# Kernel tuning notes

Measured on AMD Instinct MI355X. Metric: run time of the kernel, lower is better.

## Reference

```python
import jax, jax.numpy as jnp
import numpy as np

B, S, D = 2, 2048, 2048
NH, NKV, HD = 16, 4, 128  # num_heads, num_key_value_heads, head_dim

def setup_inputs() -> dict:
    key = jax.random.key(0)
    ks = jax.random.split(key, 5)
    sc = 0.02
    return {
        "hidden_states": jax.random.normal(ks[0], (B, S, D), jnp.float32),
        "Wq": jax.random.normal(ks[1], (NH * HD, D), jnp.float32) * sc,
        "Wk": jax.random.normal(ks[2], (NKV * HD, D), jnp.float32) * sc,
        "Wv": jax.random.normal(ks[3], (NKV * HD, D), jnp.float32) * sc,
        "Wo": jax.random.normal(ks[4], (D, NH * HD), jnp.float32) * sc,
    }

def reference(hidden_states, Wq, Wk, Wv, Wo):
    b, s, d = hidden_states.shape
    # projections (LLaMA linear: x @ W.T)
    q = jnp.einsum('bsd,ed->bse', hidden_states, Wq).reshape(b, s, NH, HD).transpose(0, 2, 1, 3)
    k = jnp.einsum('bsd,ed->bse', hidden_states, Wk).reshape(b, s, NKV, HD).transpose(0, 2, 1, 3)
    v = jnp.einsum('bsd,ed->bse', hidden_states, Wv).reshape(b, s, NKV, HD).transpose(0, 2, 1, 3)
    # GQA: repeat kv heads
    n_rep = NH // NKV
    k = jnp.repeat(k, n_rep, axis=1)  # [b, NH, s, HD]
    v = jnp.repeat(v, n_rep, axis=1)
    scale = 1.0 / jnp.sqrt(jnp.asarray(HD, hidden_states.dtype))
    scores = jnp.einsum('bhqd,bhkd->bhqk', q, k) * scale
    causal = jnp.tril(jnp.ones((s, s), bool))
    scores = jnp.where(causal, scores, jnp.asarray(-jnp.inf, scores.dtype))
    attn = jax.nn.softmax(scores, axis=-1)
    out = jnp.einsum('bhqk,bhkd->bhqd', attn, v)  # [b, NH, s, HD]
    out = out.transpose(0, 2, 1, 3).reshape(b, s, NH * HD)
    return jnp.einsum('bse,de->bsd', out, Wo)
```

## Files before the change

kernel.cpp:

```cpp
#include <hip/hip_runtime.h>

typedef unsigned short u16;
typedef unsigned int u32;
typedef __attribute__((ext_vector_type(4))) float f32x4;
typedef __attribute__((ext_vector_type(16))) float f32x16;
typedef __attribute__((ext_vector_type(8))) short bf16x8;


__device__ __forceinline__ u16 f2b(float f) {
  u32 u = __builtin_bit_cast(u32, f);
  u = (u + 0x7fffu + ((u >> 16) & 1u)) >> 16;
  return (u16)u;
}

__device__ __forceinline__ void gload_lds16(const void* g, void* l) {
  __builtin_amdgcn_global_load_lds((const __attribute__((address_space(1))) u32*)g,
                                   (__attribute__((address_space(3))) u32*)l, 16, 0, 0);
}

#if __has_builtin(__builtin_amdgcn_permlane32_swap)
#define HAS_PLS 1
__device__ __forceinline__ void pls(u32 x, u32 y, u32& rx, u32& ry) {
  auto r = __builtin_amdgcn_permlane32_swap(x, y, false, false);
  rx = (u32)r[0];
  ry = (u32)r[1];
}
#endif

__device__ __forceinline__ float xhalf_max(float v) {
#ifdef HAS_PLS
  u32 a, b;
  pls(__builtin_bit_cast(u32, v), __builtin_bit_cast(u32, v), a, b);
  return fmaxf(__builtin_bit_cast(float, a), __builtin_bit_cast(float, b));
#else
  return fmaxf(v, __shfl_xor(v, 32));
#endif
}

__device__ __forceinline__ float xhalf_sum(float v) {
#ifdef HAS_PLS
  u32 a, b;
  pls(__builtin_bit_cast(u32, v), __builtin_bit_cast(u32, v), a, b);
  return __builtin_bit_cast(float, a) + __builtin_bit_cast(float, b);
#else
  return v + __shfl_xor(v, 32);
#endif
}

__device__ __forceinline__ void xexchange(int hi, u32 a0, u32 a1, u32 a2, u32 a3, u32* o) {
#ifdef HAS_PLS
  pls(a0, a2, o[0], o[2]);
  pls(a1, a3, o[1], o[3]);
#else
  u32 xa0 = (u32)__shfl_xor((int)a0, 32), xa1 = (u32)__shfl_xor((int)a1, 32);
  u32 xa2 = (u32)__shfl_xor((int)a2, 32), xa3 = (u32)__shfl_xor((int)a3, 32);
  o[0] = hi ? xa2 : a0;
  o[1] = hi ? xa3 : a1;
  o[2] = hi ? a2 : xa0;
  o[3] = hi ? a3 : xa1;
#endif
}

__device__ __forceinline__ u32 pktrunc(float lo, float hif) {
  return (__builtin_bit_cast(u32, lo) >> 16) | (__builtin_bit_cast(u32, hif) & 0xffff0000u);
}

__global__ void cvt_bf16(const float* __restrict__ src, u16* __restrict__ dst, int n) {
  int stride = gridDim.x * blockDim.x * 4;
  for (int idx = (blockIdx.x * blockDim.x + threadIdx.x) * 4; idx < n; idx += stride) {
    float4 v = *(const float4*)(src + idx);
    ushort4 o;
    o.x = f2b(v.x); o.y = f2b(v.y); o.z = f2b(v.z); o.w = f2b(v.w);
    *(ushort4*)(dst + idx) = o;
  }
}

__global__ void cvt_w4(const float* __restrict__ Wq, const float* __restrict__ Wk,
                       const float* __restrict__ Wv, const float* __restrict__ Wo,
                       u16* __restrict__ dst) {
  const int total = 10485760;
  int stride = gridDim.x * blockDim.x * 4;
  for (int idx = (blockIdx.x * blockDim.x + threadIdx.x) * 4; idx < total; idx += stride) {
    const float* src;
    int off;
    if (idx < 4194304) { src = Wq; off = idx; }
    else if (idx < 5242880) { src = Wk; off = idx - 4194304; }
    else if (idx < 6291456) { src = Wv; off = idx - 5242880; }
    else { src = Wo; off = idx - 6291456; }
    float4 v = *(const float4*)(src + off);
    ushort4 o;
    o.x = f2b(v.x); o.y = f2b(v.y); o.z = f2b(v.z); o.w = f2b(v.w);
    *(ushort4*)(dst + idx) = o;
  }
}

template<int OUT_MODE>
__global__ __launch_bounds__(256) void gemm_bt(const u16* __restrict__ A, const u16* __restrict__ B,
                                               void* __restrict__ Cout, int M, int N, int Kd,
                                               u16* __restrict__ Kout, u16* __restrict__ Vtout) {
  __shared__ u16 smem[(OUT_MODE == 3) ? 16384 : 8192];
  u16* sA = smem;
  u16* sB = smem + 4096;
  const int tid = threadIdx.x;
  const int l = tid & 63, w = tid >> 6;
  const int wr = w >> 1, wc = w & 1;
  const int g = l >> 4, c = l & 15;
  const int tm = blockIdx.y * 128, tn = blockIdx.x * 128;

  f32x4 acc[4][4] = {};

  const int r0 = tid >> 2, cc = (tid & 3) << 3;

  for (int k0 = 0; k0 < Kd; k0 += 32) {
    __syncthreads();
    {
      const u16* srcA0 = A + (size_t)(tm + r0) * Kd + k0 + cc;
      const u16* srcB0 = B + (size_t)(tn + r0) * Kd + k0 + cc;
      gload_lds16(srcA0, (char*)sA + w * 1024);
      gload_lds16(srcB0, (char*)sB + w * 1024);
      gload_lds16(srcA0 + (size_t)64 * Kd, (char*)sA + 4096 + w * 1024);
      gload_lds16(srcB0 + (size_t)64 * Kd, (char*)sB + 4096 + w * 1024);
    }
    __syncthreads();

    bf16x8 af[4], bfr[4];
#pragma unroll
    for (int m = 0; m < 4; ++m)
      af[m] = *(const bf16x8*)(sA + (wr * 64 + m * 16 + c) * 32 + g * 8);
#pragma unroll
    for (int n = 0; n < 4; ++n)
      bfr[n] = *(const bf16x8*)(sB + (wc * 64 + n * 16 + c) * 32 + g * 8);
#pragma unroll
    for (int m = 0; m < 4; ++m)
#pragma unroll
      for (int n = 0; n < 4; ++n)
        acc[m][n] = __builtin_amdgcn_mfma_f32_16x16x32_bf16(af[m], bfr[n], acc[m][n], 0, 0, 0);
  }

  if constexpr (OUT_MODE == 3) {
    if (tn >= 2048) {
      const bool isK = tn < 2560;
      __syncthreads();
#pragma unroll
      for (int m = 0; m < 4; ++m)
#pragma unroll
        for (int n = 0; n < 4; ++n)
#pragma unroll
          for (int i = 0; i < 4; ++i) {
            int lr = wr * 64 + m * 16 + g * 4 + i;
            int lc = wc * 64 + n * 16 + c;
            int off;
            if (isK)
              off = ((lr >> 5) << 12) + ((lc >> 4) << 9) + (((lc >> 3) & 1) << 8) +
                    ((lr & 31) << 3) + (lc & 7);
            else
              off = ((lr >> 5) << 12) + (((lr >> 4) & 1) << 11) + ((lc >> 5) << 9) +
                    (((lr >> 3) & 1) << 8) + ((lc & 31) << 3) + (lr & 7);
            smem[off] = f2b(acc[m][n][i]);
          }
      __syncthreads();
      const int e0 = tn - (isK ? 2048 : 2560);
      const int bb = tm >> 11;
      u16* dstbase = (isK ? Kout : Vtout) +
                     ((((size_t)(bb * 4 + (e0 >> 7)) * 64 + ((tm & 2047) >> 5))) << 12);
#pragma unroll
      for (int ps = 0; ps < 8; ++ps) {
        int idx = ps * 2048 + tid * 8;
        *(bf16x8*)(dstbase + idx) = *(const bf16x8*)(smem + idx);
      }
      return;
    }
  }

#pragma unroll
  for (int m = 0; m < 4; ++m)
#pragma unroll
    for (int n = 0; n < 4; ++n)
#pragma unroll
      for (int i = 0; i < 4; ++i) {
        int row = tm + wr * 64 + m * 16 + g * 4 + i;
        int col = tn + wc * 64 + n * 16 + c;
        float v = acc[m][n][i];
        if constexpr (OUT_MODE == 2) {
          ((float*)Cout)[(size_t)row * N + col] = v;
        } else {
          ((u16*)Cout)[(size_t)row * 2048 + col] = f2b(v);
        }
      }
}

__global__ __launch_bounds__(256, 2) void attn_fwd(const u16* __restrict__ Q, const u16* __restrict__ Kf,
                                                   const u16* __restrict__ Vf, u16* __restrict__ AO) {
  const int l = threadIdx.x & 63, w = threadIdx.x >> 6;
  const int ql = l & 31, hi = l >> 5;
  const int bh = blockIdx.y;
  const int b = bh >> 4, h = bh & 15;
  const int kvh = h >> 2;

  __shared__ float4 mO[2][16][64];
  __shared__ float mML[2][2][64];

  const float sm = 0.08838834764831845f * 1.4426950408889634f;

  const u16* Kfb = Kf + (size_t)(b * 4 + kvh) * 64 * 4096 + l * 8;
  const u16* Vfb = Vf + (size_t)(b * 4 + kvh) * 64 * 4096 + l * 8;

  const int x = (int)blockIdx.x;

#define LOADK(KF, KV0)                                                        \
  do {                                                                        \
    const u16* kb_ = Kfb + (size_t)((KV0) >> 5) * 4096;                       \
    _Pragma("unroll") for (int ck = 0; ck < 8; ++ck)                          \
        KF[ck] = *(const bf16x8*)(kb_ + ck * 512);                            \
  } while (0)

#define COMPUTE(KF, KV0)                                                      \
  do {                                                                        \
    bf16x8 vtf[2][4];                                                         \
    {                                                                         \
      const u16* vb_ = Vfb + (size_t)((KV0) >> 5) * 4096;                     \
      _Pragma("unroll") for (int ks = 0; ks < 2; ++ks)                        \
      _Pragma("unroll") for (int db = 0; db < 4; ++db)                        \
          vtf[ks][db] = *(const bf16x8*)(vb_ + (ks * 4 + db) * 512);          \
    }                                                                         \
    f32x16 sacc = {};                                                         \
    __builtin_amdgcn_s_setprio(1);                                            \
    _Pragma("unroll") for (int ck = 0; ck < 8; ++ck)                          \
        sacc = __builtin_amdgcn_mfma_f32_32x32x16_bf16(KF[ck], qf[ck], sacc, 0, 0, 0); \
    __builtin_amdgcn_s_setprio(0);                                            \
    if ((KV0) == q0) {                             \
      _Pragma("unroll") for (int r = 0; r < 16; ++r) {                        \
        int crow = (r & 3) + 8 * (r >> 2) + 4 * hi;                           \
        if (crow > ql) sacc[r] = -1e30f;                                      \
      }                                                                       \
    }                                                                         \
    float t0 = fmaxf(sacc[0], sacc[1]), t1 = fmaxf(sacc[2], sacc[3]);         \
    float t2 = fmaxf(sacc[4], sacc[5]), t3 = fmaxf(sacc[6], sacc[7]);         \
    float t4 = fmaxf(sacc[8], sacc[9]), t5 = fmaxf(sacc[10], sacc[11]);       \
    float t6 = fmaxf(sacc[12], sacc[13]), t7 = fmaxf(sacc[14], sacc[15]);     \
    float mx = fmaxf(fmaxf(fmaxf(t0, t1), fmaxf(t2, t3)),                     \
                     fmaxf(fmaxf(t4, t5), fmaxf(t6, t7)));                    \
    mx = xhalf_max(mx);                                                       \
    float p[16];                                                              \
    _Pragma("unroll") for (int r = 0; r < 16; ++r)                            \
        p[r] = exp2f((sacc[r] - mrow) * sm);                                  \
    if (!__all((mx - mrow) * sm <= 8.0f)) {                \
      float mnew = fmaxf(mrow, mx);                                           \
      float rs = exp2f((mrow - mnew) * sm);                                   \
      mrow = mnew;                                                            \
      lrow *= rs;                                                             \
      _Pragma("unroll") for (int db = 0; db < 4; ++db)                        \
      _Pragma("unroll") for (int r = 0; r < 16; ++r) acc[db][r] *= rs;        \
      _Pragma("unroll") for (int r = 0; r < 16; ++r)                          \
          p[r] = exp2f((sacc[r] - mrow) * sm);                                \
    }                                                                         \
    float s0 = p[0] + p[1], s1 = p[2] + p[3], s2 = p[4] + p[5], s3 = p[6] + p[7]; \
    float s4 = p[8] + p[9], s5 = p[10] + p[11], s6 = p[12] + p[13], s7 = p[14] + p[15]; \
    float psum = ((s0 + s1) + (s2 + s3)) + ((s4 + s5) + (s6 + s7));           \
    lrow += xhalf_sum(psum);                                                  \
    u32 a0 = pktrunc(p[0], p[1]), a1 = pktrunc(p[2], p[3]);                   \
    u32 a2 = pktrunc(p[4], p[5]), a3 = pktrunc(p[6], p[7]);                   \
    u32 b0 = pktrunc(p[8], p[9]), b1 = pktrunc(p[10], p[11]);                 \
    u32 b2 = pktrunc(p[12], p[13]), b3 = pktrunc(p[14], p[15]);               \
    union { bf16x8 v; u32 u[4]; } pa0, pa1;                                   \
    xexchange(hi, a0, a1, a2, a3, pa0.u);                                     \
    xexchange(hi, b0, b1, b2, b3, pa1.u);                                     \
    __builtin_amdgcn_s_setprio(1);                                            \
    _Pragma("unroll") for (int db = 0; db < 4; ++db) {                        \
      acc[db] = __builtin_amdgcn_mfma_f32_32x32x16_bf16(vtf[0][db], pa0.v, acc[db], 0, 0, 0); \
      acc[db] = __builtin_amdgcn_mfma_f32_32x32x16_bf16(vtf[1][db], pa1.v, acc[db], 0, 0, 0); \
    }                                                                         \
    __builtin_amdgcn_s_setprio(0);                                            \
  } while (0)

#define PUBLISH(SLOT)                                                         \
  do {                                                                        \
    _Pragma("unroll") for (int db = 0; db < 4; ++db)                          \
    _Pragma("unroll") for (int rq = 0; rq < 4; ++rq) {                        \
      float4 v;                                                               \
      v.x = acc[db][rq * 4 + 0];                                              \
      v.y = acc[db][rq * 4 + 1];                                              \
      v.z = acc[db][rq * 4 + 2];                                              \
      v.w = acc[db][rq * 4 + 3];                                              \
      mO[SLOT][db * 4 + rq][l] = v;                                           \
    }                                                                         \
    mML[SLOT][0][l] = mrow;                                                   \
    mML[SLOT][1][l] = lrow;                                                   \
  } while (0)

#define MERGE(SLOT)                                                           \
  do {                                                                        \
    float m1 = mML[SLOT][0][l], l1 = mML[SLOT][1][l];                         \
    float mnew = fmaxf(mrow, m1);                                             \
    float f0 = exp2f((mrow - mnew) * sm);                                     \
    float f1 = exp2f((m1 - mnew) * sm);                                       \
    mrow = mnew;                                                              \
    lrow = lrow * f0 + l1 * f1;                                               \
    _Pragma("unroll") for (int db = 0; db < 4; ++db)                          \
    _Pragma("unroll") for (int rq = 0; rq < 4; ++rq) {                        \
      float4 o1 = mO[SLOT][db * 4 + rq][l];                                   \
      acc[db][rq * 4 + 0] = acc[db][rq * 4 + 0] * f0 + o1.x * f1;             \
      acc[db][rq * 4 + 1] = acc[db][rq * 4 + 1] * f0 + o1.y * f1;             \
      acc[db][rq * 4 + 2] = acc[db][rq * 4 + 2] * f0 + o1.z * f1;             \
      acc[db][rq * 4 + 3] = acc[db][rq * 4 + 3] * f0 + o1.w * f1;             \
    }                                                                         \
  } while (0)

  for (int phase = 0; phase < 2; ++phase) {
    const int t = phase ? (63 - x) : x;
    const int q0 = t * 32;

    bf16x8 qf[8];
    {
      const u16* qb = Q + ((size_t)(b * 2048 + q0 + ql)) * 2048 + h * 128 + hi * 8;
#pragma unroll
      for (int ck = 0; ck < 8; ++ck) qf[ck] = *(const bf16x8*)(qb + ck * 16);
    }

    f32x16 acc[4] = {};
    float mrow = -1e30f, lrow = 0.f;

    bf16x8 kfa[8], kfb[8];

    int kv0 = w * 32;
    if (kv0 <= q0) {
      LOADK(kfa, kv0);
      while (true) {
        bool more = kv0 + 128 <= q0;
        if (more) LOADK(kfb, kv0 + 128);
        COMPUTE(kfa, kv0);
        if (!more) break;
        kv0 += 128;
        more = kv0 + 128 <= q0;
        if (more) LOADK(kfa, kv0 + 128);
        COMPUTE(kfb, kv0);
        if (!more) break;
        kv0 += 128;
      }
    }

    if (w >= 2) PUBLISH(w - 2);
    __syncthreads();
    if (w < 2) MERGE(w);
    __syncthreads();
    if (w == 1) PUBLISH(0);
    __syncthreads();
    if (w == 0) {
      MERGE(0);
      float inv = 1.0f / lrow;
      u16* ob = AO + (size_t)(b * 2048 + q0 + ql) * 2048 + h * 128 + hi * 4;
#pragma unroll
      for (int db = 0; db < 4; ++db)
#pragma unroll
        for (int rq = 0; rq < 4; ++rq) {
          ushort4 o;
          o.x = f2b(acc[db][rq * 4 + 0] * inv);
          o.y = f2b(acc[db][rq * 4 + 1] * inv);
          o.z = f2b(acc[db][rq * 4 + 2] * inv);
          o.w = f2b(acc[db][rq * 4 + 3] * inv);
          *(ushort4*)(ob + db * 32 + rq * 8) = o;
        }
    }
    __syncthreads();
  }
#undef LOADK
#undef COMPUTE
#undef PUBLISH
#undef MERGE
}

extern "C" void kernel_launch(void* const* d_in, const int* in_sizes, int n_in,
                              void* d_out, int out_size, void* d_ws, size_t ws_size,
                              hipStream_t stream) {
  const float* X = (const float*)d_in[0];
  const float* Wq = (const float*)d_in[1];
  const float* Wk = (const float*)d_in[2];
  const float* Wv = (const float*)d_in[3];
  const float* Wo = (const float*)d_in[4];

  u16* ws = (u16*)d_ws;
  const size_t nX = 8388608;
  const size_t nWq = 4194304;
  const size_t nWk = 1048576;
  u16* Xb = ws;
  u16* Wqb = Xb + nX;
  u16* Wkb = Wqb + nWq;
  u16* Wvb = Wkb + nWk;
  u16* Wob = Wvb + nWk;
  u16* Qb = Wob + nWq;
  u16* Kfb = Qb + nX;
  u16* Vfb = Kfb + 2097152;
  u16* AOb = Vfb + 2097152;
  if (ws_size < (size_t)(39845888) * 2) return;

  cvt_bf16<<<2048, 256, 0, stream>>>(X, Xb, (int)nX);
  cvt_w4<<<2048, 256, 0, stream>>>(Wq, Wk, Wv, Wo, Wqb);

  gemm_bt<3><<<dim3(24, 32), 256, 0, stream>>>(Xb, Wqb, Qb, 4096, 3072, 2048, Kfb, Vfb);

  attn_fwd<<<dim3(32, 32), 256, 0, stream>>>(Qb, Kfb, Vfb, AOb);

  gemm_bt<2><<<dim3(16, 32), 256, 0, stream>>>(AOb, Wob, d_out, 4096, 2048, 2048, nullptr, nullptr);
}
```

Measured before the change: 216.4 us.

## Replace GEMMs with 256x256-tile double-buffered swizzled-LDS kernel

```diff
diff --git a/kernel.cpp b/kernel.cpp
--- a/kernel.cpp
+++ b/kernel.cpp
@@ -95,98 +95,149 @@
 }
 
 template<int OUT_MODE>
-__global__ __launch_bounds__(256) void gemm_bt(const u16* __restrict__ A, const u16* __restrict__ B,
+__global__ __launch_bounds__(512) void gemm256(const u16* __restrict__ A, const u16* __restrict__ B,
                                                void* __restrict__ Cout, int M, int N, int Kd,
-                                               u16* __restrict__ Kout, u16* __restrict__ Vtout) {
-  __shared__ u16 smem[(OUT_MODE == 3) ? 16384 : 8192];
-  u16* sA = smem;
-  u16* sB = smem + 4096;
+                                               u16* __restrict__ Kout, u16* __restrict__ Vout) {
+  __shared__ u16 smem[65536];
   const int tid = threadIdx.x;
   const int l = tid & 63, w = tid >> 6;
-  const int wr = w >> 1, wc = w & 1;
-  const int g = l >> 4, c = l & 15;
-  const int tm = blockIdx.y * 128, tn = blockIdx.x * 128;
-
-  f32x4 acc[4][4] = {};
-
-  const int r0 = tid >> 2, cc = (tid & 3) << 3;
-
-  for (int k0 = 0; k0 < Kd; k0 += 32) {
-    __syncthreads();
-    {
-      const u16* srcA0 = A + (size_t)(tm + r0) * Kd + k0 + cc;
-      const u16* srcB0 = B + (size_t)(tn + r0) * Kd + k0 + cc;
-      gload_lds16(srcA0, (char*)sA + w * 1024);
-      gload_lds16(srcB0, (char*)sB + w * 1024);
-      gload_lds16(srcA0 + (size_t)64 * Kd, (char*)sA + 4096 + w * 1024);
-      gload_lds16(srcB0 + (size_t)64 * Kd, (char*)sB + 4096 + w * 1024);
-    }
-    __syncthreads();
-
-    bf16x8 af[4], bfr[4];
-#pragma unroll
-    for (int m = 0; m < 4; ++m)
-      af[m] = *(const bf16x8*)(sA + (wr * 64 + m * 16 + c) * 32 + g * 8);
+  const int c = l & 15, g = l >> 4;
+  const int wr = w >> 2, wc = w & 3;
+  const int tm = blockIdx.y * 256, tn = blockIdx.x * 256;
+
+  const int lr = tid >> 3;
+  const int lcol = (tid & 7) * 8;
+  const int scol = lcol ^ (((lr >> 1) & 3) << 4);
+  const int swc = ((c >> 1) & 3) << 4;
+
+#define BARX() do { __builtin_amdgcn_s_barrier(); asm volatile("" ::: "memory"); } while (0)
+#define STG(SRC, GROW0, LDS0) \
+  gload_lds16((SRC) + (size_t)((GROW0) + lr) * Kd + k0n + scol, (LDS0) + lr * 64 + lcol)
+
+  f32x4 acc[8][4] = {};
+
+  {
+    const int k0n = 0;
+    u16* sAn = smem;
+    u16* sBn = smem + 16384;
+    STG(B, tn + 0, sBn); STG(B, tn + 64, sBn + 64 * 64);
+    STG(B, tn + 128, sBn + 128 * 64); STG(B, tn + 192, sBn + 192 * 64);
+    STG(A, tm + 0, sAn); STG(A, tm + 128, sAn + 128 * 64);
+    STG(A, tm + 64, sAn + 64 * 64); STG(A, tm + 192, sAn + 192 * 64);
+  }
+
+  const int nt = Kd >> 6;
+  for (int t = 0; t < nt; ++t) {
+    const int slot = t & 1;
+    u16* sAc = smem + slot * 32768;
+    u16* sBc = sAc + 16384;
+    u16* sAn = smem + (slot ^ 1) * 32768;
+    u16* sBn = sAn + 16384;
+    const int k0n = (t + 1) << 6;
+    const bool st = (t + 1) < nt;
+
+    bf16x8 bfr[4][2], af[2][2];
+
+#define APH(q)                                                                  \
+  do {                                                                          \
+    _Pragma("unroll") for (int m2 = 0; m2 < 2; ++m2)                            \
+    _Pragma("unroll") for (int kk = 0; kk < 2; ++kk)                            \
+        af[m2][kk] = *(const bf16x8*)(sAc + (wr * 128 + (q) * 32 + m2 * 16 + c) * 64 + \
+                                      ((kk * 32 + g * 8) ^ swc));               \
+    __builtin_amdgcn_s_setprio(1);                                              \
+    _Pragma("unroll") for (int m2 = 0; m2 < 2; ++m2)                            \
+    _Pragma("unroll") for (int n = 0; n < 4; ++n)                               \
+    _Pragma("unroll") for (int kk = 0; kk < 2; ++kk)                            \
+        acc[(q) * 2 + m2][n] = __builtin_amdgcn_mfma_f32_16x16x32_bf16(         \
+            af[m2][kk], bfr[n][kk], acc[(q) * 2 + m2][n], 0, 0, 0);             \
+    __builtin_amdgcn_s_setprio(0);                                              \
+  } while (0)
+
+    BARX();
+    if (st) { STG(B, tn + 0, sBn); STG(B, tn + 64, sBn + 64 * 64); }
+    if (st) asm volatile("s_waitcnt vmcnt(4)" ::: "memory");
+    else    asm volatile("s_waitcnt vmcnt(2)" ::: "memory");
+    BARX();
 #pragma unroll
     for (int n = 0; n < 4; ++n)
-      bfr[n] = *(const bf16x8*)(sB + (wc * 64 + n * 16 + c) * 32 + g * 8);
-#pragma unroll
-    for (int m = 0; m < 4; ++m)
-#pragma unroll
-      for (int n = 0; n < 4; ++n)
-        acc[m][n] = __builtin_amdgcn_mfma_f32_16x16x32_bf16(af[m], bfr[n], acc[m][n], 0, 0, 0);
+#pragma unroll
+      for (int kk = 0; kk < 2; ++kk)
+        bfr[n][kk] = *(const bf16x8*)(sBc + (wc * 64 + n * 16 + c) * 64 +
+                                      ((kk * 32 + g * 8) ^ swc));
+    APH(0);
+    if (st) { STG(B, tn + 128, sBn + 128 * 64); STG(B, tn + 192, sBn + 192 * 64); }
+    APH(1);
+    if (st) { STG(A, tm + 0, sAn); STG(A, tm + 128, sAn + 128 * 64); }
+    if (st) asm volatile("s_waitcnt vmcnt(6)" ::: "memory");
+    else    asm volatile("s_waitcnt vmcnt(0)" ::: "memory");
+    BARX();
+    APH(2);
+    if (st) { STG(A, tm + 64, sAn + 64 * 64); STG(A, tm + 192, sAn + 192 * 64); }
+    APH(3);
+#undef APH
   }
 
   if constexpr (OUT_MODE == 3) {
     if (tn >= 2048) {
       const bool isK = tn < 2560;
-      __syncthreads();
-#pragma unroll
-      for (int m = 0; m < 4; ++m)
+      BARX();
+#pragma unroll
+      for (int mi = 0; mi < 8; ++mi)
 #pragma unroll
         for (int n = 0; n < 4; ++n)
 #pragma unroll
           for (int i = 0; i < 4; ++i) {
-            int lr = wr * 64 + m * 16 + g * 4 + i;
-            int lc = wc * 64 + n * 16 + c;
+            int s = wr * 128 + (mi >> 1) * 32 + (mi & 1) * 16 + g * 4 + i;
+            int e = wc * 64 + n * 16 + c;
+            int chunk = (e >> 7) * 8 + (s >> 5);
             int off;
-            if (isK)
-              off = ((lr >> 5) << 12) + ((lc >> 4) << 9) + (((lc >> 3) & 1) << 8) +
-                    ((lr & 31) << 3) + (lc & 7);
-            else
-              off = ((lr >> 5) << 12) + (((lr >> 4) & 1) << 11) + ((lc >> 5) << 9) +
-                    (((lr >> 3) & 1) << 8) + ((lc & 31) << 3) + (lr & 7);
-            smem[off] = f2b(acc[m][n][i]);
+            if (isK) {
+              int k = e & 127;
+              off = chunk * 4096 + (k >> 4) * 512 + ((k >> 3) & 1) * 256 + (s & 31) * 8 + (k & 7);
+            } else {
+              int d = e & 127;
+              off = chunk * 4096 + (((s >> 4) & 1) * 4 + (d >> 5)) * 512 + ((s >> 3) & 1) * 256 +
+                    (d & 31) * 8 + (s & 7);
+            }
+            smem[off] = f2b(acc[mi][n][i]);
           }
-      __syncthreads();
-      const int e0 = tn - (isK ? 2048 : 2560);
+      BARX();
+      const int kvh_base = (tn - (isK ? 2048 : 2560)) >> 7;
       const int bb = tm >> 11;
-      u16* dstbase = (isK ? Kout : Vtout) +
-                     ((((size_t)(bb * 4 + (e0 >> 7)) * 64 + ((tm & 2047) >> 5))) << 12);
-#pragma unroll
-      for (int ps = 0; ps < 8; ++ps) {
-        int idx = ps * 2048 + tid * 8;
-        *(bf16x8*)(dstbase + idx) = *(const bf16x8*)(smem + idx);
+      const int kvt0 = (tm & 2047) >> 5;
+      u16* Out = isK ? Kout : Vout;
+#pragma unroll
+      for (int ch = 0; ch < 16; ++ch) {
+        u16* dst = Out + (size_t)((bb * 4 + kvh_base + (ch >> 3)) * 64 + kvt0 + (ch & 7)) * 4096;
+        *(bf16x8*)(dst + tid * 8) = *(const bf16x8*)(smem + ch * 4096 + tid * 8);
       }
       return;
     }
-  }
-
-#pragma unroll
-  for (int m = 0; m < 4; ++m)
+#pragma unroll
+    for (int mi = 0; mi < 8; ++mi)
+#pragma unroll
+      for (int n = 0; n < 4; ++n)
+#pragma unroll
+        for (int i = 0; i < 4; ++i) {
+          int row = tm + wr * 128 + (mi >> 1) * 32 + (mi & 1) * 16 + g * 4 + i;
+          int col = tn + wc * 64 + n * 16 + c;
+          ((u16*)Cout)[(size_t)row * 2048 + col] = f2b(acc[mi][n][i]);
+        }
+    return;
+  }
+
+#pragma unroll
+  for (int mi = 0; mi < 8; ++mi)
 #pragma unroll
     for (int n = 0; n < 4; ++n)
 #pragma unroll
       for (int i = 0; i < 4; ++i) {
-        int row = tm + wr * 64 + m * 16 + g * 4 + i;
+        int row = tm + wr * 128 + (mi >> 1) * 32 + (mi & 1) * 16 + g * 4 + i;
         int col = tn + wc * 64 + n * 16 + c;
-        float v = acc[m][n][i];
-        if constexpr (OUT_MODE == 2) {
-          ((float*)Cout)[(size_t)row * N + col] = v;
-        } else {
-          ((u16*)Cout)[(size_t)row * 2048 + col] = f2b(v);
-        }
+        ((float*)Cout)[(size_t)row * N + col] = acc[mi][n][i];
       }
+#undef STG
+#undef BARX
 }
 
 __global__ __launch_bounds__(256, 2) void attn_fwd(const u16* __restrict__ Q, const u16* __restrict__ Kf,
@@ -396,9 +447,9 @@
   cvt_bf16<<<2048, 256, 0, stream>>>(X, Xb, (int)nX);
   cvt_w4<<<2048, 256, 0, stream>>>(Wq, Wk, Wv, Wo, Wqb);
 
-  gemm_bt<3><<<dim3(24, 32), 256, 0, stream>>>(Xb, Wqb, Qb, 4096, 3072, 2048, Kfb, Vfb);
+  gemm256<3><<<dim3(12, 16), 512, 0, stream>>>(Xb, Wqb, Qb, 4096, 3072, 2048, Kfb, Vfb);
 
   attn_fwd<<<dim3(32, 32), 256, 0, stream>>>(Qb, Kfb, Vfb, AOb);
 
-  gemm_bt<2><<<dim3(16, 32), 256, 0, stream>>>(AOb, Wob, d_out, 4096, 2048, 2048, nullptr, nullptr);
-}
+  gemm256<2><<<dim3(8, 16), 512, 0, stream>>>(AOb, Wob, d_out, 4096, 2048, 2048, nullptr, nullptr);
+}
```

After: 198.9 us. 1.09x faster.
